# Performance work log

Hardware: AMD Instinct MI355X
Metric: run time of the kernel (lower is better)

## Reference

```python
import jax, jax.numpy as jnp
import numpy as np

GRAPH_SIZE = 1024
D_MODEL = 256
BATCH = 32
INITIAL_ALPHA = 1.0


def setup_inputs() -> dict:
    key = jax.random.key(0)
    ks = jax.random.split(key, 10)
    s = 1.0 / np.sqrt(D_MODEL)  # torch Linear default init scale
    inp = {
        "query": jax.random.normal(ks[0], (BATCH, GRAPH_SIZE, D_MODEL), jnp.float32),
        "key_": jax.random.normal(ks[1], (BATCH, GRAPH_SIZE, D_MODEL), jnp.float32),
        "value": jax.random.normal(ks[2], (BATCH, GRAPH_SIZE, D_MODEL), jnp.float32),
        "dist": jax.random.uniform(ks[3], (BATCH, GRAPH_SIZE, GRAPH_SIZE), jnp.float32),
        "Wq": jax.random.uniform(ks[4], (D_MODEL, D_MODEL), jnp.float32, -s, s),
        "bq": jax.random.uniform(ks[5], (D_MODEL,), jnp.float32, -s, s),
        "Wk": jax.random.uniform(ks[6], (D_MODEL, D_MODEL), jnp.float32, -s, s),
        "bk": jax.random.uniform(ks[7], (D_MODEL,), jnp.float32, -s, s),
        "Wv": jax.random.uniform(ks[8], (D_MODEL, D_MODEL), jnp.float32, -s, s),
        "bv": jax.random.uniform(ks[9], (D_MODEL,), jnp.float32, -s, s),
        # alpha_raw = exp(initial_alpha - 1)
        "alpha_raw": jnp.asarray(np.exp(INITIAL_ALPHA - 1.0), jnp.float32),
    }
    return inp


def reference(query, key_, value, dist, Wq, bq, Wk, bk, Wv, bv, alpha_raw):
    # self-attention path: mask=None, cross=False, query_size == graph_size
    log2_N = jnp.log2(jnp.asarray(GRAPH_SIZE, jnp.float32))
    alpha = jax.nn.softplus(alpha_raw) + 1e-6

    q = jnp.einsum('bnd,ed->bne', query, Wq) + bq   # fc_q
    k = jnp.einsum('bnd,ed->bne', key_, Wk) + bk    # fc_k
    v = jnp.einsum('bnd,ed->bne', value, Wv) + bv   # fc_v

    exp_A = jnp.exp(-alpha * log2_N * dist)         # [b, n, n]
    exp_K = jnp.exp(k)                              # [b, n, d]

    numerator = jnp.einsum('bqk,bkd->bqd', exp_A, exp_K * v)
    denominator = jnp.einsum('bqk,bkd->bqd', exp_A, exp_K) + 1e-8
    return jax.nn.sigmoid(q) * (numerator / denominator)
```

## Files before the change

### kernel.cpp

```cpp
#include <hip/hip_runtime.h>
#include <hip/hip_bf16.h>

#define NBATCH 32
#define NG 1024
#define DM 256

typedef short bf16x8 __attribute__((ext_vector_type(8)));
typedef float f32x4 __attribute__((ext_vector_type(4)));
typedef unsigned short u16x4 __attribute__((ext_vector_type(4)));
typedef unsigned short u16x8 __attribute__((ext_vector_type(8)));

static __device__ __forceinline__ unsigned short f2bf(float f) {
    __hip_bfloat16 h = __float2bfloat16(f);
    return *reinterpret_cast<unsigned short*>(&h);
}
static __device__ __forceinline__ float bf2f(unsigned short u) {
    unsigned int x = ((unsigned int)u) << 16;
    return *reinterpret_cast<float*>(&x);
}

static __device__ __forceinline__ void gload16(const void* g, void* l) {
    __builtin_amdgcn_global_load_lds(
        (const __attribute__((address_space(1))) unsigned int*)g,
        (__attribute__((address_space(3))) unsigned int*)l, 16, 0, 0);
}

static __device__ __forceinline__ void wait_vm8_bar() {
    asm volatile("s_waitcnt vmcnt(8)" ::: "memory");
    asm volatile("s_barrier" ::: "memory");
    __builtin_amdgcn_sched_barrier(0);
}
static __device__ __forceinline__ void wait_vm4_bar() {
    asm volatile("s_waitcnt vmcnt(4)" ::: "memory");
    asm volatile("s_barrier" ::: "memory");
    __builtin_amdgcn_sched_barrier(0);
}
static __device__ __forceinline__ void wait_vm0_bar() {
    asm volatile("s_waitcnt vmcnt(0)" ::: "memory");
    asm volatile("s_barrier" ::: "memory");
    __builtin_amdgcn_sched_barrier(0);
}
static __device__ __forceinline__ void bar_only() {
    asm volatile("s_barrier" ::: "memory");
}

__global__ __launch_bounds__(256) void wpack_kernel(
    const float* __restrict__ Wq, const float* __restrict__ Wk,
    const float* __restrict__ Wv, unsigned short* __restrict__ Wb)
{
    const int i4 = (blockIdx.x * 256 + threadIdx.x) * 4;
    const int t = i4 >> 16;
    const int off = i4 & 65535;
    const float* src = (t == 0) ? Wq : (t == 1) ? Wk : Wv;
    float4 v = *(const float4*)(src + off);
    *(u16x4*)(Wb + i4) = (u16x4){ f2bf(v.x), f2bf(v.y), f2bf(v.z), f2bf(v.w) };
}

__global__ __launch_bounds__(256) void conv3_kernel(
    const float* __restrict__ q, const float* __restrict__ k,
    const float* __restrict__ v, unsigned short* __restrict__ Xb)
{
    const int sel = blockIdx.x >> 12;
    const float* src = (sel == 0) ? q : (sel == 1) ? k : v;
    const size_t i8 = (((size_t)(blockIdx.x & 4095)) * 256 + threadIdx.x) * 8;
    float4 a = *(const float4*)(src + i8);
    float4 b = *(const float4*)(src + i8 + 4);
    *(u16x8*)(Xb + (size_t)sel * NBATCH * NG * DM + i8) =
        (u16x8){ f2bf(a.x), f2bf(a.y), f2bf(a.z), f2bf(a.w),
                 f2bf(b.x), f2bf(b.y), f2bf(b.z), f2bf(b.w) };
}

__global__ __launch_bounds__(256) void exp_kernel(
    const float* __restrict__ dist, unsigned short* __restrict__ ea,
    const float* __restrict__ alpha_raw)
{
    const float alpha = log1pf(__expf(alpha_raw[0])) + 1e-6f;
    const float sc = -alpha * 10.0f * 1.44269504088896f;
    const size_t i8 = ((size_t)blockIdx.x * 256 + threadIdx.x) * 8;
    float4 v0 = *(const float4*)(dist + i8);
    float4 v1 = *(const float4*)(dist + i8 + 4);
    u16x8 o = { f2bf(exp2f(sc * v0.x)), f2bf(exp2f(sc * v0.y)),
                f2bf(exp2f(sc * v0.z)), f2bf(exp2f(sc * v0.w)),
                f2bf(exp2f(sc * v1.x)), f2bf(exp2f(sc * v1.y)),
                f2bf(exp2f(sc * v1.z)), f2bf(exp2f(sc * v1.w)) };
    *(u16x8*)(ea + i8) = o;
}

__global__ __launch_bounds__(256) void projq_kernel(
    const unsigned short* __restrict__ Xq,
    const unsigned short* __restrict__ Wb,
    const float* __restrict__ bq,
    unsigned short* __restrict__ qb)
{
    __shared__ __align__(128) unsigned short lds[2][2][128 * 64];

    const int bid = blockIdx.x;
    const int mt = bid >> 1, nt = bid & 1;
    const int tid = threadIdx.x;
    const int w = tid >> 6, lane = tid & 63;
    const int wm = w >> 1, wn = w & 1;
    const int l15 = lane & 15, lhi = lane >> 4;
    const int lr = lane >> 3, sl = lane & 7;
    const int sp = sl ^ lr;

    const char* Abase = (const char*)(Xq + (size_t)mt * 128 * 256);
    const char* Wbase = (const char*)(Wb + (size_t)nt * 128 * 256);

    f32x4 acc[4][4];
    #pragma unroll
    for (int mi = 0; mi < 4; ++mi)
        #pragma unroll
        for (int ni = 0; ni < 4; ++ni)
            acc[mi][ni] = (f32x4){0.f, 0.f, 0.f, 0.f};

    auto STAGE = [&](int buf, int t) {
        #pragma unroll
        for (int i = 0; i < 4; ++i) {
            const int r = w * 32 + i * 8 + lr;
            gload16(Abase + (size_t)r * 512 + t * 128 + sp * 16,
                    (char*)&lds[buf][0][0] + w * 4096 + i * 1024);
            gload16(Wbase + (size_t)r * 512 + t * 128 + sp * 16,
                    (char*)&lds[buf][1][0] + w * 4096 + i * 1024);
        }
    };

    STAGE(0, 0);
    int cur = 0;
    for (int t = 0; t < 4; ++t) {
        if (t < 3) { STAGE(cur ^ 1, t + 1); wait_vm8_bar(); }
        else       { wait_vm0_bar(); }
        const char* Ab = (const char*)&lds[cur][0][0];
        const char* Bb = (const char*)&lds[cur][1][0];
        #pragma unroll
        for (int kk = 0; kk < 2; ++kk) {
            bf16x8 af[4], bfr[4];
            #pragma unroll
            for (int mi = 0; mi < 4; ++mi) {
                const int tr = wm * 64 + mi * 16 + l15;
                af[mi] = *(const bf16x8*)(Ab + ((tr * 128 + kk * 64 + lhi * 16) ^ ((tr & 7) << 4)));
            }
            #pragma unroll
            for (int ni = 0; ni < 4; ++ni) {
                const int tr = wn * 64 + ni * 16 + l15;
                bfr[ni] = *(const bf16x8*)(Bb + ((tr * 128 + kk * 64 + lhi * 16) ^ ((tr & 7) << 4)));
            }
            #pragma unroll
            for (int mi = 0; mi < 4; ++mi)
                #pragma unroll
                for (int ni = 0; ni < 4; ++ni)
                    acc[mi][ni] = __builtin_amdgcn_mfma_f32_16x16x32_bf16(
                        af[mi], bfr[ni], acc[mi][ni], 0, 0, 0);
        }
        bar_only();
        cur ^= 1;
    }

    #pragma unroll
    for (int ni = 0; ni < 4; ++ni) {
        const int c = nt * 128 + wn * 64 + ni * 16 + l15;
        const float bqs = bq[c];
        #pragma unroll
        for (int mi = 0; mi < 4; ++mi)
            #pragma unroll
            for (int r = 0; r < 4; ++r) {
                const size_t R = (size_t)mt * 128 + wm * 64 + mi * 16 + lhi * 4 + r;
                qb[R * DM + c] = f2bf(acc[mi][ni][r] + bqs);
            }
    }
}

__global__ __launch_bounds__(256) void projkv_kernel(
    const unsigned short* __restrict__ Xk,
    const unsigned short* __restrict__ Xv,
    const unsigned short* __restrict__ Wkb,
    const unsigned short* __restrict__ Wvb,
    const float* __restrict__ bk, const float* __restrict__ bv,
    unsigned short* __restrict__ Pt)
{
    __shared__ __align__(128) unsigned short lds[2][2][128 * 64];

    const int bid = blockIdx.x;
    const int mt = bid >> 1, nt = bid & 1;
    const int tid = threadIdx.x;
    const int w = tid >> 6, lane = tid & 63;
    const int wm = w >> 1, wn = w & 1;
    const int l15 = lane & 15, lhi = lane >> 4;
    const int lr = lane >> 3, sl = lane & 7;
    const int sp = sl ^ lr;
    const int g16 = (sp & 3) * 16;

    f32x4 kacc[4][4], vacc[4][4];
    #pragma unroll
    for (int mi = 0; mi < 4; ++mi)
        #pragma unroll
        for (int ni = 0; ni < 4; ++ni) {
            kacc[mi][ni] = (f32x4){0.f, 0.f, 0.f, 0.f};
            vacc[mi][ni] = (f32x4){0.f, 0.f, 0.f, 0.f};
        }

    auto STAGE = [&](int buf, int t) {
        #pragma unroll
        for (int i = 0; i < 4; ++i) {
            const int r = w * 32 + i * 8 + lr;
            const char* asrc = (sp < 4 ? (const char*)Xk : (const char*)Xv)
                               + (size_t)(mt * 128 + r) * 512 + t * 64 + g16;
            gload16(asrc, (char*)&lds[buf][0][0] + w * 4096 + i * 1024);
            const char* wsrc = (sp < 4 ? (const char*)Wkb : (const char*)Wvb)
                               + (size_t)(nt * 128 + r) * 512 + t * 64 + g16;
            gload16(wsrc, (char*)&lds[buf][1][0] + w * 4096 + i * 1024);
        }
    };

    STAGE(0, 0);
    int cur = 0;
    for (int t = 0; t < 8; ++t) {
        if (t < 7) { STAGE(cur ^ 1, t + 1); wait_vm8_bar(); }
        else       { wait_vm0_bar(); }
        const char* Ab = (const char*)&lds[cur][0][0];
        const char* Bb = (const char*)&lds[cur][1][0];
        bf16x8 kaf[4], vaf[4], kbf[4], vbf[4];
        #pragma unroll
        for (int mi = 0; mi < 4; ++mi) {
            const int tr = wm * 64 + mi * 16 + l15;
            const int sw = (tr & 7) << 4;
            kaf[mi] = *(const bf16x8*)(Ab + ((tr * 128 + lhi * 16) ^ sw));
            vaf[mi] = *(const bf16x8*)(Ab + ((tr * 128 + 64 + lhi * 16) ^ sw));
        }
        #pragma unroll
        for (int ni = 0; ni < 4; ++ni) {
            const int tr = wn * 64 + ni * 16 + l15;
            const int sw = (tr & 7) << 4;
            kbf[ni] = *(const bf16x8*)(Bb + ((tr * 128 + lhi * 16) ^ sw));
            vbf[ni] = *(const bf16x8*)(Bb + ((tr * 128 + 64 + lhi * 16) ^ sw));
        }
        #pragma unroll
        for (int mi = 0; mi < 4; ++mi)
            #pragma unroll
            for (int ni = 0; ni < 4; ++ni) {
                kacc[mi][ni] = __builtin_amdgcn_mfma_f32_16x16x32_bf16(
                    kaf[mi], kbf[ni], kacc[mi][ni], 0, 0, 0);
                vacc[mi][ni] = __builtin_amdgcn_mfma_f32_16x16x32_bf16(
                    vaf[mi], vbf[ni], vacc[mi][ni], 0, 0, 0);
            }
        bar_only();
        cur ^= 1;
    }

    const int b = (mt * 128) >> 10;
    const int kb0 = (mt * 128) & 1023;
    #pragma unroll
    for (int ni = 0; ni < 4; ++ni) {
        const int c = nt * 128 + wn * 64 + ni * 16 + l15;
        const float bks = bk[c], bvs = bv[c];
        #pragma unroll
        for (int mi = 0; mi < 4; ++mi) {
            unsigned short p1[4], p2[4];
            #pragma unroll
            for (int r = 0; r < 4; ++r) {
                const float ek = __expf(kacc[mi][ni][r] + bks);
                const float vv = vacc[mi][ni][r] + bvs;
                p1[r] = f2bf(ek * vv);
                p2[r] = f2bf(ek);
            }
            const int kidx = kb0 + wm * 64 + mi * 16 + lhi * 4;
            *(u16x4*)&Pt[((size_t)b * 512 + 2 * c    ) * NG + kidx] =
                (u16x4){p1[0], p1[1], p1[2], p1[3]};
            *(u16x4*)&Pt[((size_t)b * 512 + 2 * c + 1) * NG + kidx] =
                (u16x4){p2[0], p2[1], p2[2], p2[3]};
        }
    }
}

__global__ __launch_bounds__(512, 2) void attn_kernel(
    const unsigned short* __restrict__ ea,
    const unsigned short* __restrict__ Pt,
    const unsigned short* __restrict__ qb,
    float* __restrict__ out)
{
    __shared__ __align__(128) char lds[4][2][16384];

    const int bid = blockIdx.x;
    const int l = (bid & 7) * 32 + (bid >> 3);
    const int b = l >> 3;
    const int m = (l >> 1) & 3;
    const int n = l & 1;

    const int tid = threadIdx.x;
    const int w = tid >> 6, lane = tid & 63;
    const int wm = w >> 2, wn = w & 3;
    const int l15 = lane & 15, lhi = lane >> 4;
    const int xv = (l15 >> 1) & 3;

    const int isB = w >> 2;
    const int sw = w & 3;
    const int srow = lane >> 2;
    const int sg = (lane & 3) ^ ((lane >> 3) & 3);

    const char* Abase = (const char*)(ea + ((size_t)b * NG + m * 256) * NG);
    const char* Bbase = (const char*)(Pt + ((size_t)b * 512 + n * 256) * NG);
    const char* Sbase = isB ? Bbase : Abase;

    f32x4 acc[8][4];
    #pragma unroll
    for (int mi = 0; mi < 8; ++mi)
        #pragma unroll
        for (int ni = 0; ni < 4; ++ni)
            acc[mi][ni] = (f32x4){0.f, 0.f, 0.f, 0.f};

    auto STAGE = [&](int slot, int t) {
        #pragma unroll
        for (int i = 0; i < 4; ++i) {
            const int r = sw * 64 + i * 16 + srow;
            gload16(Sbase + (size_t)r * 2048 + t * 64 + sg * 16,
                    &lds[slot][isB][0] + sw * 4096 + i * 1024);
        }
    };

    STAGE(0, 0);
    STAGE(1, 1);
    for (int t = 0; t < 32; ++t) {
        if (t < 30)      { STAGE((t + 2) & 3, t + 2); wait_vm8_bar(); }
        else if (t == 30){ wait_vm4_bar(); }
        else             { wait_vm0_bar(); }
        const char* Ab = &lds[t & 3][0][0];
        const char* Bb = &lds[t & 3][1][0];
        __builtin_amdgcn_s_setprio(1);
        bf16x8 af[8], bfr[4];
        #pragma unroll
        for (int mi = 0; mi < 8; ++mi) {
            const int tr = wm * 128 + mi * 16 + l15;
            af[mi] = *(const bf16x8*)(Ab + tr * 64 + ((lhi ^ xv) * 16));
        }
        #pragma unroll
        for (int ni = 0; ni < 4; ++ni) {
            const int tr = wn * 64 + ni * 16 + l15;
            bfr[ni] = *(const bf16x8*)(Bb + tr * 64 + ((lhi ^ xv) * 16));
        }
        #pragma unroll
        for (int mi = 0; mi < 8; ++mi)
            #pragma unroll
            for (int ni = 0; ni < 4; ++ni)
                acc[mi][ni] = __builtin_amdgcn_mfma_f32_16x16x32_bf16(
                    af[mi], bfr[ni], acc[mi][ni], 0, 0, 0);
        __builtin_amdgcn_s_setprio(0);
    }

    const int parity = lane & 1;
    #pragma unroll
    for (int mi = 0; mi < 8; ++mi)
        #pragma unroll
        for (int ni = 0; ni < 4; ++ni)
            #pragma unroll
            for (int r = 0; r < 4; ++r) {
                const float own = acc[mi][ni][r];
                const float other = __shfl_xor(own, 1, 64);
                if (!parity) {
                    const int colg = n * 256 + wn * 64 + ni * 16 + l15;
                    const int d = colg >> 1;
                    const int rowg = m * 256 + wm * 128 + mi * 16 + lhi * 4 + r;
                    const size_t idx = ((size_t)b * NG + rowg) * DM + d;
                    const float q = bf2f(qb[idx]);
                    const float sig = 1.0f / (1.0f + __expf(-q));
                    out[idx] = sig * (own / (other + 1e-8f));
                }
            }
}

extern "C" void kernel_launch(void* const* d_in, const int* in_sizes, int n_in,
                              void* d_out, int out_size, void* d_ws, size_t ws_size,
                              hipStream_t stream) {
    const float* query = (const float*)d_in[0];
    const float* key_  = (const float*)d_in[1];
    const float* value = (const float*)d_in[2];
    const float* dist  = (const float*)d_in[3];
    const float* Wq = (const float*)d_in[4];
    const float* bq = (const float*)d_in[5];
    const float* Wk = (const float*)d_in[6];
    const float* bk = (const float*)d_in[7];
    const float* Wv = (const float*)d_in[8];
    const float* bv = (const float*)d_in[9];
    const float* alpha_raw = (const float*)d_in[10];
    float* out = (float*)d_out;

    unsigned short* Pt = (unsigned short*)d_ws;
    unsigned short* ea = Pt + (size_t)NBATCH * 512 * NG;
    unsigned short* Xb = ea + (size_t)NBATCH * NG * NG;
    const size_t XN = (size_t)NBATCH * NG * DM;
    unsigned short* qb = Xb + 3 * XN;
    unsigned short* Wb = qb + XN;

    wpack_kernel<<<dim3(192), dim3(256), 0, stream>>>(Wq, Wk, Wv, Wb);
    conv3_kernel<<<dim3(12288), dim3(256), 0, stream>>>(query, key_, value, Xb);

    projq_kernel<<<dim3(512), dim3(256), 0, stream>>>(Xb, Wb, bq, qb);
    projkv_kernel<<<dim3(512), dim3(256), 0, stream>>>(
        Xb + XN, Xb + 2 * XN, Wb + 65536, Wb + 131072, bk, bv, Pt);

    exp_kernel<<<dim3(16384), dim3(256), 0, stream>>>(dist, ea, alpha_raw);
    attn_kernel<<<dim3(256), dim3(512), 0, stream>>>(ea, Pt, qb, out);
}
```

Measured before the change: 187.5 us.

## Restructure attention GEMM main loop into 8-wave ping-pong schedule with 64-wide K tiles

Replaces the 4-slot, 32-element-K ring buffer with double-buffered 64-element-K tiles split into half-tiles. Global-to-LDS loads are interleaved between quarter-MFMA blocks, separated by barriers and explicit lgkmcnt/vmcnt waits. The LDS layout moves to 128-byte rows with an XOR swizzle on the row index. The aim is to overlap loads with MFMA more finely and cut per-iteration sync overhead, at the cost of many more barriers and a tricky buffer-reuse schedule that could race or stall.

Measured after the change: 192.9 us. +2.9%, slower.

```diff
diff --git a/kernel.cpp b/kernel.cpp
--- a/kernel.cpp
+++ b/kernel.cpp
@@ -27,11 +27,6 @@
 
 static __device__ __forceinline__ void wait_vm8_bar() {
     asm volatile("s_waitcnt vmcnt(8)" ::: "memory");
-    asm volatile("s_barrier" ::: "memory");
-    __builtin_amdgcn_sched_barrier(0);
-}
-static __device__ __forceinline__ void wait_vm4_bar() {
-    asm volatile("s_waitcnt vmcnt(4)" ::: "memory");
     asm volatile("s_barrier" ::: "memory");
     __builtin_amdgcn_sched_barrier(0);
 }
@@ -277,7 +272,7 @@
     const unsigned short* __restrict__ qb,
     float* __restrict__ out)
 {
-    __shared__ __align__(128) char lds[4][2][16384];
+    __shared__ __align__(128) char lds[2][2][2][128 * 128];
 
     const int bid = blockIdx.x;
     const int l = (bid & 7) * 32 + (bid >> 3);
@@ -289,16 +284,12 @@
     const int w = tid >> 6, lane = tid & 63;
     const int wm = w >> 2, wn = w & 3;
     const int l15 = lane & 15, lhi = lane >> 4;
-    const int xv = (l15 >> 1) & 3;
-
-    const int isB = w >> 2;
-    const int sw = w & 3;
-    const int srow = lane >> 2;
-    const int sg = (lane & 3) ^ ((lane >> 3) & 3);
+
+    const int srow = tid >> 3;
+    const int sg = (tid & 7) ^ (srow & 7);
 
     const char* Abase = (const char*)(ea + ((size_t)b * NG + m * 256) * NG);
     const char* Bbase = (const char*)(Pt + ((size_t)b * 512 + n * 256) * NG);
-    const char* Sbase = isB ? Bbase : Abase;
 
     f32x4 acc[8][4];
     #pragma unroll
@@ -307,43 +298,115 @@
         for (int ni = 0; ni < 4; ++ni)
             acc[mi][ni] = (f32x4){0.f, 0.f, 0.f, 0.f};
 
-    auto STAGE = [&](int slot, int t) {
-        #pragma unroll
-        for (int i = 0; i < 4; ++i) {
-            const int r = sw * 64 + i * 16 + srow;
-            gload16(Sbase + (size_t)r * 2048 + t * 64 + sg * 16,
-                    &lds[slot][isB][0] + sw * 4096 + i * 1024);
-        }
-    };
-
-    STAGE(0, 0);
-    STAGE(1, 1);
-    for (int t = 0; t < 32; ++t) {
-        if (t < 30)      { STAGE((t + 2) & 3, t + 2); wait_vm8_bar(); }
-        else if (t == 30){ wait_vm4_bar(); }
-        else             { wait_vm0_bar(); }
-        const char* Ab = &lds[t & 3][0][0];
-        const char* Bb = &lds[t & 3][1][0];
+    bf16x8 af[8];
+    bf16x8 bfr[8];
+
+    auto UNIT = [&](int buf, int op, int h, int t) {
+        const char* S = op ? Bbase : Abase;
+        char* D = &lds[buf][op][h][0] + w * 1024;
+        #pragma unroll
+        for (int j = 0; j < 2; ++j) {
+            const int r = h * 128 + j * 64 + srow;
+            gload16(S + (size_t)r * 2048 + (size_t)(t & 15) * 128 + sg * 16,
+                    D + j * 8192);
+        }
+    };
+    auto RD_A = [&](int buf, int mh) {
+        const char* Ah = &lds[buf][0][wm][0];
+        #pragma unroll
+        for (int q = 0; q < 4; ++q) {
+            const int row = (mh * 4 + q) * 16 + l15;
+            #pragma unroll
+            for (int kk = 0; kk < 2; ++kk)
+                af[q * 2 + kk] = *(const bf16x8*)(
+                    Ah + ((row * 128 + kk * 64 + lhi * 16) ^ ((row & 7) << 4)));
+        }
+    };
+    auto RD_B = [&](int buf) {
+        const char* Bh = &lds[buf][1][wn >> 1][0];
+        #pragma unroll
+        for (int ni = 0; ni < 4; ++ni) {
+            const int row = (wn & 1) * 64 + ni * 16 + l15;
+            #pragma unroll
+            for (int kk = 0; kk < 2; ++kk)
+                bfr[ni * 2 + kk] = *(const bf16x8*)(
+                    Bh + ((row * 128 + kk * 64 + lhi * 16) ^ ((row & 7) << 4)));
+        }
+    };
+    auto QMFMA = [&](int mh, int nh) {
         __builtin_amdgcn_s_setprio(1);
-        bf16x8 af[8], bfr[4];
-        #pragma unroll
-        for (int mi = 0; mi < 8; ++mi) {
-            const int tr = wm * 128 + mi * 16 + l15;
-            af[mi] = *(const bf16x8*)(Ab + tr * 64 + ((lhi ^ xv) * 16));
-        }
-        #pragma unroll
-        for (int ni = 0; ni < 4; ++ni) {
-            const int tr = wn * 64 + ni * 16 + l15;
-            bfr[ni] = *(const bf16x8*)(Bb + tr * 64 + ((lhi ^ xv) * 16));
-        }
-        #pragma unroll
-        for (int mi = 0; mi < 8; ++mi)
-            #pragma unroll
-            for (int ni = 0; ni < 4; ++ni)
-                acc[mi][ni] = __builtin_amdgcn_mfma_f32_16x16x32_bf16(
-                    af[mi], bfr[ni], acc[mi][ni], 0, 0, 0);
+        #pragma unroll
+        for (int q = 0; q < 4; ++q)
+            #pragma unroll
+            for (int nj = 0; nj < 2; ++nj)
+                #pragma unroll
+                for (int kk = 0; kk < 2; ++kk)
+                    acc[mh * 4 + q][nh * 2 + nj] = __builtin_amdgcn_mfma_f32_16x16x32_bf16(
+                        af[q * 2 + kk], bfr[(nh * 2 + nj) * 2 + kk],
+                        acc[mh * 4 + q][nh * 2 + nj], 0, 0, 0);
         __builtin_amdgcn_s_setprio(0);
-    }
+    };
+    auto LGK0 = [&]() {
+        asm volatile("s_waitcnt lgkmcnt(0)" ::: "memory");
+        __builtin_amdgcn_sched_barrier(0);
+    };
+
+    #pragma unroll
+    for (int u = 0; u < 4; ++u) {
+        UNIT(0, u >> 1, u & 1, 0);
+        UNIT(1, u >> 1, u & 1, 1);
+    }
+    asm volatile("s_waitcnt vmcnt(0)" ::: "memory");
+    __builtin_amdgcn_s_barrier();
+
+    for (int i = 0; i < 8; ++i) {
+        const int Tb = 2 * i + 1;
+        RD_A(0, 0); RD_B(0);
+        UNIT(1, 0, 1, Tb);
+        __builtin_amdgcn_s_barrier();
+        LGK0();
+        QMFMA(0, 0);
+        __builtin_amdgcn_s_barrier();
+        UNIT(0, 1, 0, Tb + 1);
+        __builtin_amdgcn_s_barrier();
+        QMFMA(0, 1);
+        __builtin_amdgcn_s_barrier();
+        RD_A(0, 1);
+        UNIT(0, 1, 1, Tb + 1);
+        __builtin_amdgcn_s_barrier();
+        LGK0();
+        QMFMA(1, 0);
+        __builtin_amdgcn_s_barrier();
+        UNIT(0, 0, 0, Tb + 1);
+        __builtin_amdgcn_s_barrier();
+        QMFMA(1, 1);
+        asm volatile("s_waitcnt vmcnt(6)" ::: "memory");
+        __builtin_amdgcn_s_barrier();
+        RD_A(1, 0); RD_B(1);
+        UNIT(0, 0, 1, Tb + 1);
+        __builtin_amdgcn_s_barrier();
+        LGK0();
+        QMFMA(0, 0);
+        __builtin_amdgcn_s_barrier();
+        UNIT(1, 1, 0, Tb + 2);
+        __builtin_amdgcn_s_barrier();
+        QMFMA(0, 1);
+        __builtin_amdgcn_s_barrier();
+        RD_A(1, 1);
+        UNIT(1, 1, 1, Tb + 2);
+        __builtin_amdgcn_s_barrier();
+        LGK0();
+        QMFMA(1, 0);
+        __builtin_amdgcn_s_barrier();
+        UNIT(1, 0, 0, Tb + 2);
+        __builtin_amdgcn_s_barrier();
+        QMFMA(1, 1);
+        asm volatile("s_waitcnt vmcnt(6)" ::: "memory");
+        __builtin_amdgcn_s_barrier();
+    }
+
+    asm volatile("s_waitcnt vmcnt(0)" ::: "memory");
+    __builtin_amdgcn_s_barrier();
 
     const int parity = lane & 1;
     #pragma unroll
```
